# Kernel tuning notes

Measured on AMD Instinct MI355X. Metric: run time of the kernel, lower is better.

Reference implementation:

```python
import math
import jax, jax.numpy as jnp
import numpy as np

B, T, C, H = 4, 2048, 1024, 16
D = C // H          # head dim 64
FF = 4 * C          # 4096

def setup_inputs() -> dict:
    key = jax.random.key(0)
    ks = jax.random.split(key, 7)
    s = 0.02
    return {
        "x":      jax.random.normal(ks[0], (B, T, C), jnp.float32),
        "g1":     jnp.ones((C,), jnp.float32),                      # ln_1 weight (bias=False)
        "w_qkv":  jax.random.normal(ks[1], (3 * C, C), jnp.float32) * s,  # torch Linear [out,in]
        "w_o":    jax.random.normal(ks[2], (C, C), jnp.float32) * s,
        "g2":     jnp.ones((C,), jnp.float32),                      # ln_2 weight
        "w_fc":   jax.random.normal(ks[3], (FF, C), jnp.float32) * s,
        "w_proj": jax.random.normal(ks[4], (C, FF), jnp.float32) * s,
    }

def _layernorm(x, g):
    mu = jnp.mean(x, axis=-1, keepdims=True)
    var = jnp.mean(jnp.square(x - mu), axis=-1, keepdims=True)
    return (x - mu) * jax.lax.rsqrt(var + 1e-5) * g

def _attn(x, w_qkv, w_o):
    qkv = x @ w_qkv.T                                  # [B,T,3C]
    q, k, v = jnp.split(qkv, 3, axis=-1)
    q = q.reshape(B, T, H, D).transpose(0, 2, 1, 3)    # [B,H,T,D]
    k = k.reshape(B, T, H, D).transpose(0, 2, 1, 3)
    v = v.reshape(B, T, H, D).transpose(0, 2, 1, 3)
    att = jnp.einsum('bhtd,bhsd->bhts', q, k) * (1.0 / math.sqrt(D))
    mask = jnp.tril(jnp.ones((T, T), bool))
    att = jnp.where(mask, att, -jnp.inf)
    att = jax.nn.softmax(att, axis=-1)
    y = jnp.einsum('bhts,bhsd->bhtd', att, v)          # [B,H,T,D]
    y = y.transpose(0, 2, 1, 3).reshape(B, T, C)
    return y @ w_o.T

def _mlp(x, w_fc, w_proj):
    h = jax.nn.gelu(x @ w_fc.T, approximate=False)     # torch nn.GELU default = exact erf
    return h @ w_proj.T

def reference(x, g1, w_qkv, w_o, g2, w_fc, w_proj):
    x = x + _attn(_layernorm(x, g1), w_qkv, w_o)
    x = x + _mlp(_layernorm(x, g2), w_fc, w_proj)
    return x
```

## Files before the change

kernel.cpp:

```cpp
#include <hip/hip_runtime.h>

typedef __attribute__((ext_vector_type(8))) short bs8;
typedef __attribute__((ext_vector_type(4))) short bs4;
typedef __attribute__((ext_vector_type(4))) float f32x4;

__device__ __forceinline__ float b2f(short u) {
  union { unsigned int i; float f; } c;
  c.i = ((unsigned int)(unsigned short)u) << 16;
  return c.f;
}
__device__ __forceinline__ unsigned short f2bs(float f) {
  union { float f; unsigned int i; } c; c.f = f;
  unsigned int r = (c.i + 0x7FFFu + ((c.i >> 16) & 1u)) >> 16;
  return (unsigned short)r;
}
__device__ __forceinline__ void async16(const void* g, void* l) {
  __builtin_amdgcn_global_load_lds((__attribute__((address_space(1))) void*)g,
                                   (__attribute__((address_space(3))) void*)l, 16, 0, 0);
}

__device__ __forceinline__ float gelu_fast(float v) {
  const float x = v * 0.70710678118654752f;
  const float ax = fabsf(x);
  const float t = 1.0f / (1.0f + 0.3275911f * ax);
  float p = 1.061405429f;
  p = p * t - 1.453152027f;
  p = p * t + 1.421413741f;
  p = p * t - 0.284496736f;
  p = p * t + 0.254829592f;
  const float e = __expf(-ax * ax);
  float er = 1.0f - p * t * e;
  er = copysignf(er, x);
  return 0.5f * v * (1.0f + er);
}

__global__ void detect_kernel(const unsigned int* __restrict__ g1raw, int* __restrict__ flag) {
  *flag = (g1raw[0] == 0x3F800000u) ? 1 : 0;
}

struct CvtArgs {
  const void* src[7];
  unsigned short* dst[7];
  int start[8];
};
__global__ __launch_bounds__(256) void cvt_all_kernel(CvtArgs a, const int* __restrict__ flag) {
  int blk = blockIdx.x;
  int seg = 0;
  #pragma unroll
  for (int s = 1; s < 7; ++s) if (blk >= a.start[s]) seg = s;
  const int i = ((blk - a.start[seg]) * 256 + threadIdx.x) * 4;
  const void* src = a.src[seg];
  unsigned short* dst = a.dst[seg];
  if (*flag) {
    const float4 t = *(const float4*)((const float*)src + i);
    bs4 o; o[0] = f2bs(t.x); o[1] = f2bs(t.y); o[2] = f2bs(t.z); o[3] = f2bs(t.w);
    *(bs4*)(dst + i) = o;
  } else {
    *(bs4*)(dst + i) = *(const bs4*)((const unsigned short*)src + i);
  }
}

__global__ __launch_bounds__(256) void ln_kernel(const unsigned short* __restrict__ xin,
                                                 const unsigned short* __restrict__ g,
                                                 unsigned short* __restrict__ out) {
  const int row = blockIdx.x;
  const int tid = threadIdx.x;
  const size_t base = (size_t)row * 1024 + tid * 4;
  float v[4];
  const bs4 t = *(const bs4*)(xin + base);
  v[0] = b2f(t[0]); v[1] = b2f(t[1]); v[2] = b2f(t[2]); v[3] = b2f(t[3]);
  float s  = v[0] + v[1] + v[2] + v[3];
  float sq = v[0]*v[0] + v[1]*v[1] + v[2]*v[2] + v[3]*v[3];
  for (int off = 32; off > 0; off >>= 1) { s += __shfl_xor(s, off); sq += __shfl_xor(sq, off); }
  __shared__ float sm[8];
  const int wv = tid >> 6;
  if ((tid & 63) == 0) { sm[wv] = s; sm[4 + wv] = sq; }
  __syncthreads();
  s  = sm[0] + sm[1] + sm[2] + sm[3];
  sq = sm[4] + sm[5] + sm[6] + sm[7];
  const float mu = s * (1.0f / 1024.0f);
  const float rstd = rsqrtf(sq * (1.0f / 1024.0f) - mu * mu + 1e-5f);
  const bs4 gt = *(const bs4*)(g + tid * 4);
  unsigned short* op = out + base;
  #pragma unroll
  for (int i = 0; i < 4; ++i) op[i] = f2bs((v[i] - mu) * rstd * b2f(gt[i]));
}

template<int EPI>
__global__ __launch_bounds__(256, 2) void gemm_bt(const unsigned short* __restrict__ X,
                                                  const unsigned short* __restrict__ W,
                                                  const unsigned short* __restrict__ res,
                                                  void* __restrict__ out,
                                                  const int* __restrict__ flagp,
                                                  int M, int N, int K) {
  __shared__ __align__(16) unsigned short Alds[2][128 * 64];
  __shared__ __align__(16) unsigned short Blds[2][128 * 64];
  const int tid  = threadIdx.x;
  const int wave = tid >> 6, lane = tid & 63;
  const int c16 = lane & 15, q8 = (lane >> 4) * 8;
  const int wm = (wave >> 1) * 64, wn = (wave & 1) * 64;

  const int nbn = gridDim.x;
  const int d = blockIdx.y * nbn + blockIdx.x;
  const int xcd = d & 7, slot = d >> 3;
  const int cpx = (nbn * gridDim.y) >> 3;
  const int sq = xcd * (cpx >> 6) + (slot >> 6);
  const int r  = slot & 63;
  const int nsx = nbn >> 3;
  const int bn = ((sq % nsx) * 8 + (r & 7)) * 128;
  const int bm = ((sq / nsx) * 8 + (r >> 3)) * 128;

  const int sw = (c16 & 7) << 4;

  int isf32 = 0;
  if constexpr (EPI == 3) isf32 = *flagp;

  f32x4 acc[4][4] = {};

  const int srow = tid >> 3;
  const int scb  = ((tid & 7) * 16) ^ ((srow & 7) << 4);

  auto STAGE = [&](int k0, int b) {
    #pragma unroll
    for (int it = 0; it < 4; ++it) {
      const int row = it * 32 + srow;
      async16((const char*)X + ((size_t)(bm + row) * K + k0) * 2 + scb,
              (char*)&Alds[b][0] + (it * 256 + tid) * 16);
      async16((const char*)W + ((size_t)(bn + row) * K + k0) * 2 + scb,
              (char*)&Blds[b][0] + (it * 256 + tid) * 16);
    }
  };

  auto COMPUTE = [&](int b) {
    const char* Ab = (const char*)&Alds[b][0];
    const char* Bb = (const char*)&Blds[b][0];
    #pragma unroll
    for (int kk = 0; kk < 64; kk += 32) {
      bs8 af[4], bf[4];
      #pragma unroll
      for (int mi = 0; mi < 4; ++mi)
        af[mi] = *(const bs8*)(Ab + (wm + mi * 16 + c16) * 128 + (((kk + q8) * 2) ^ sw));
      #pragma unroll
      for (int ni = 0; ni < 4; ++ni)
        bf[ni] = *(const bs8*)(Bb + (wn + ni * 16 + c16) * 128 + (((kk + q8) * 2) ^ sw));
      #pragma unroll
      for (int mi = 0; mi < 4; ++mi)
        #pragma unroll
        for (int ni = 0; ni < 4; ++ni)
          acc[mi][ni] = __builtin_amdgcn_mfma_f32_16x16x32_bf16(af[mi], bf[ni], acc[mi][ni], 0, 0, 0);
    }
  };

  STAGE(0, 0);
  int cur = 0;
  for (int k0 = 0; k0 < K - 64; k0 += 64) {
    STAGE(k0 + 64, cur ^ 1);
    asm volatile("s_waitcnt vmcnt(8)" ::: "memory");
    __builtin_amdgcn_s_barrier();
    COMPUTE(cur);
    __builtin_amdgcn_s_barrier();
    cur ^= 1;
  }
  asm volatile("s_waitcnt vmcnt(0)" ::: "memory");
  __builtin_amdgcn_s_barrier();
  COMPUTE(cur);

  const int q4 = (lane >> 4) * 4;
  #pragma unroll
  for (int mi = 0; mi < 4; ++mi) {
    #pragma unroll
    for (int r2 = 0; r2 < 4; ++r2) {
      const size_t row = bm + wm + mi * 16 + q4 + r2;
      #pragma unroll
      for (int ni = 0; ni < 4; ++ni) {
        const size_t col = bn + wn + ni * 16 + c16;
        const size_t idx = row * (size_t)N + col;
        float v = acc[mi][ni][r2];
        if constexpr (EPI == 0) {
          ((unsigned short*)out)[idx] = f2bs(v);
        } else if constexpr (EPI == 1) {
          ((unsigned short*)out)[idx] = f2bs(gelu_fast(v));
        } else if constexpr (EPI == 2) {
          v += b2f(res[idx]);
          ((unsigned short*)out)[idx] = f2bs(v);
        } else {
          v += b2f(res[idx]);
          if (isf32) ((float*)out)[idx] = v;
          else       ((unsigned short*)out)[idx] = f2bs(v);
        }
      }
    }
  }
}

__global__ __launch_bounds__(256) void vtrans_kernel(const unsigned short* __restrict__ qkv,
                                                     unsigned short* __restrict__ vt) {
  constexpr int T = 2048, C3 = 3072;
  __shared__ __align__(16) unsigned short tile[64][72];
  const int tid = threadIdx.x;
  const int t0 = blockIdx.x * 64;
  const int bh = blockIdx.y; const int b = bh >> 4, h = bh & 15;
  const int r = tid >> 3, c = (tid & 7) * 8;
  #pragma unroll
  for (int it = 0; it < 2; ++it) {
    const int t = it * 32 + r;
    *(bs8*)&tile[t][c] = *(const bs8*)(qkv + ((size_t)(b * T + t0 + t)) * C3 + 2048 + h * 64 + c);
  }
  __syncthreads();
  #pragma unroll
  for (int it = 0; it < 2; ++it) {
    const int d = it * 32 + r;
    bs8 o;
    #pragma unroll
    for (int j = 0; j < 8; ++j) o[j] = (short)tile[c + j][d];
    *(bs8*)(vt + ((size_t)bh * 64 + d) * T + t0 + c) = o;
  }
}

struct KF { bs8 a[4][2]; };

__device__ __forceinline__ void ldsFrag(KF& f, const char* buf, int c16, int quad) {
  const int sw = (c16 & 7) << 4;
  #pragma unroll
  for (int g = 0; g < 4; ++g) {
    const int rowb = (g * 16 + c16) * 128 + quad * 16;
    f.a[g][0] = *(const bs8*)(buf + ((rowb) ^ sw));
    f.a[g][1] = *(const bs8*)(buf + ((rowb + 64) ^ sw));
  }
}

template<bool DO_A, bool MA, bool MB>
__device__ __forceinline__ void tile2(const char* Kb, const char* Vb, int kvbase,
                                      const bs8& qfA0, const bs8& qfA1,
                                      const bs8& qfB0, const bs8& qfB1,
                                      f32x4 (&oA)[4], f32x4 (&oB)[4],
                                      float (&lsA)[4], float (&lsB)[4],
                                      char* Pw, int qrowA, int qrowB,
                                      int c16, int quad) {
  KF kf, vf;
  ldsFrag(kf, Kb, c16, quad);
  ldsFrag(vf, Vb, c16, quad);

  f32x4 sA[4], sB[4];
  #pragma unroll
  for (int g = 0; g < 4; ++g) {
    if constexpr (DO_A) {
      f32x4 z = {};
      z = __builtin_amdgcn_mfma_f32_16x16x32_bf16(qfA0, kf.a[g][0], z, 0, 0, 0);
      sA[g] = __builtin_amdgcn_mfma_f32_16x16x32_bf16(qfA1, kf.a[g][1], z, 0, 0, 0);
    }
    f32x4 z2 = {};
    z2 = __builtin_amdgcn_mfma_f32_16x16x32_bf16(qfB0, kf.a[g][0], z2, 0, 0, 0);
    sB[g] = __builtin_amdgcn_mfma_f32_16x16x32_bf16(qfB1, kf.a[g][1], z2, 0, 0, 0);
  }

  #pragma unroll
  for (int r = 0; r < 4; ++r) {
    const int prow = quad * 4 + r;
    const int pbase = prow * 128;
    const int psw = (prow & 7) << 4;
    #pragma unroll
    for (int g = 0; g < 4; ++g) {
      const int col2 = (g * 16 + c16) * 2;
      if constexpr (DO_A) {
        float p = __expf(sA[g][r] * 0.125f - 4.0f);
        if constexpr (MA) { if (kvbase + g * 16 + c16 > qrowA + r) p = 0.f; }
        lsA[r] += p;
        *(unsigned short*)(Pw + ((pbase + col2) ^ psw)) = f2bs(p);
      }
      float p2 = __expf(sB[g][r] * 0.125f - 4.0f);
      if constexpr (MB) { if (kvbase + g * 16 + c16 > qrowB + r) p2 = 0.f; }
      lsB[r] += p2;
      *(unsigned short*)(Pw + 2048 + ((pbase + col2) ^ psw)) = f2bs(p2);
    }
  }
  asm volatile("s_waitcnt lgkmcnt(0)" ::: "memory");

  const int rsw = (c16 & 7) << 4;
  const int rbase = c16 * 128 + quad * 16;
  bs8 pA0, pA1;
  if constexpr (DO_A) {
    pA0 = *(const bs8*)(Pw + ((rbase) ^ rsw));
    pA1 = *(const bs8*)(Pw + ((rbase + 64) ^ rsw));
  }
  const bs8 pB0 = *(const bs8*)(Pw + 2048 + ((rbase) ^ rsw));
  const bs8 pB1 = *(const bs8*)(Pw + 2048 + ((rbase + 64) ^ rsw));
  #pragma unroll
  for (int g = 0; g < 4; ++g) {
    if constexpr (DO_A) {
      oA[g] = __builtin_amdgcn_mfma_f32_16x16x32_bf16(pA0, vf.a[g][0], oA[g], 0, 0, 0);
      oA[g] = __builtin_amdgcn_mfma_f32_16x16x32_bf16(pA1, vf.a[g][1], oA[g], 0, 0, 0);
    }
    oB[g] = __builtin_amdgcn_mfma_f32_16x16x32_bf16(pB0, vf.a[g][0], oB[g], 0, 0, 0);
    oB[g] = __builtin_amdgcn_mfma_f32_16x16x32_bf16(pB1, vf.a[g][1], oB[g], 0, 0, 0);
  }
}

__global__ __launch_bounds__(256) void attn_kernel(const unsigned short* __restrict__ qkv,
                                                   const unsigned short* __restrict__ vt,
                                                   unsigned short* __restrict__ y) {
  constexpr int T = 2048, C3 = 3072, CC = 1024;
  __shared__ __align__(16) unsigned short Klds[2][4096];
  __shared__ __align__(16) unsigned short Vlds[2][4096];
  __shared__ __align__(16) unsigned short Plds[4][2048];

  const int tid = threadIdx.x;
  const int wv = tid >> 6, lane = tid & 63;
  const int quad = lane >> 4, c16 = lane & 15;
  const int bh = blockIdx.x;
  const int b = bh >> 4, h = bh & 15;
  const int i = blockIdx.y;
  const int qA = i, qB = 31 - i;
  const size_t rowbase = (size_t)b * T;
  char* Pw = (char*)&Plds[wv][0];

  const int y0 = tid * 16, y1 = 4096 + tid * 16;
  const int r0 = y0 >> 7, r1 = y1 >> 7;
  const int s0 = y0 ^ ((r0 & 7) << 4);
  const int s1 = y1 ^ ((r1 & 7) << 4);
  const char* Ksrc0 = (const char*)qkv + ((size_t)(b * T) + r0) * 6144 + 2048 + h * 128 + (s0 & 127);
  const char* Ksrc1 = (const char*)qkv + ((size_t)(b * T) + r1) * 6144 + 2048 + h * 128 + (s1 & 127);
  const char* Vsrc0 = (const char*)vt + ((size_t)bh * 64 + r0) * (T * 2) + (s0 & 127);
  const char* Vsrc1 = (const char*)vt + ((size_t)bh * 64 + r1) * (T * 2) + (s1 & 127);

  auto STAGE = [&](int kt, int buf) {
    char* Kb = (char*)&Klds[buf][0];
    char* Vb = (char*)&Vlds[buf][0];
    const size_t ko = (size_t)kt * (64 * 6144);
    const int vo = kt * 128;
    async16(Ksrc0 + ko, Kb + y0);
    async16(Ksrc1 + ko, Kb + y1);
    async16(Vsrc0 + vo, Vb + y0);
    async16(Vsrc1 + vo, Vb + y1);
  };

  STAGE(0, 0);

  bs8 qfA0, qfA1, qfB0, qfB1;
  {
    const unsigned short* qpA = qkv + (rowbase + qA * 64 + wv * 16 + c16) * C3 + h * 64 + quad * 8;
    qfA0 = *(const bs8*)qpA; qfA1 = *(const bs8*)(qpA + 32);
    const unsigned short* qpB = qkv + (rowbase + qB * 64 + wv * 16 + c16) * C3 + h * 64 + quad * 8;
    qfB0 = *(const bs8*)qpB; qfB1 = *(const bs8*)(qpB + 32);
  }
  const int qrowA = qA * 64 + wv * 16 + quad * 4;
  const int qrowB = qB * 64 + wv * 16 + quad * 4;

  f32x4 oA[4] = {}, oB[4] = {};
  float lsA[4] = {}, lsB[4] = {};

  __syncthreads();

  int cur = 0, kt = 0;
  for (; kt < qA; ++kt) {
    STAGE(kt + 1, cur ^ 1);
    tile2<true, false, false>((const char*)&Klds[cur][0], (const char*)&Vlds[cur][0], kt * 64,
                              qfA0, qfA1, qfB0, qfB1, oA, oB, lsA, lsB, Pw, qrowA, qrowB, c16, quad);
    __syncthreads(); cur ^= 1;
  }
  STAGE(kt + 1, cur ^ 1);
  tile2<true, true, false>((const char*)&Klds[cur][0], (const char*)&Vlds[cur][0], kt * 64,
                           qfA0, qfA1, qfB0, qfB1, oA, oB, lsA, lsB, Pw, qrowA, qrowB, c16, quad);
  __syncthreads(); cur ^= 1; ++kt;
  for (; kt < qB; ++kt) {
    STAGE(kt + 1, cur ^ 1);
    tile2<false, false, false>((const char*)&Klds[cur][0], (const char*)&Vlds[cur][0], kt * 64,
                               qfA0, qfA1, qfB0, qfB1, oA, oB, lsA, lsB, Pw, qrowA, qrowB, c16, quad);
    __syncthreads(); cur ^= 1;
  }
  tile2<false, false, true>((const char*)&Klds[cur][0], (const char*)&Vlds[cur][0], kt * 64,
                            qfA0, qfA1, qfB0, qfB1, oA, oB, lsA, lsB, Pw, qrowA, qrowB, c16, quad);

  #pragma unroll
  for (int r = 0; r < 4; ++r) {
    for (int off = 1; off < 16; off <<= 1) {
      lsA[r] += __shfl_xor(lsA[r], off);
      lsB[r] += __shfl_xor(lsB[r], off);
    }
  }

  #pragma unroll
  for (int r = 0; r < 4; ++r) {
    const float invA = 1.0f / lsA[r];
    unsigned short* ypA = y + (rowbase + qrowA + r) * CC + h * 64 + c16;
    ypA[0]  = f2bs(oA[0][r] * invA);
    ypA[16] = f2bs(oA[1][r] * invA);
    ypA[32] = f2bs(oA[2][r] * invA);
    ypA[48] = f2bs(oA[3][r] * invA);
    const float invB = 1.0f / lsB[r];
    unsigned short* ypB = y + (rowbase + qrowB + r) * CC + h * 64 + c16;
    ypB[0]  = f2bs(oB[0][r] * invB);
    ypB[16] = f2bs(oB[1][r] * invB);
    ypB[32] = f2bs(oB[2][r] * invB);
    ypB[48] = f2bs(oB[3][r] * invB);
  }
}

extern "C" void kernel_launch(void* const* d_in, const int* in_sizes, int n_in,
                              void* d_out, int out_size, void* d_ws, size_t ws_size,
                              hipStream_t stream) {
  char* ws = (char*)d_ws;
  unsigned short* xc     = (unsigned short*)(ws);
  unsigned short* wqkvc  = (unsigned short*)(ws + 16777216);
  unsigned short* woc    = (unsigned short*)(ws + 23068672);
  unsigned short* wfcc   = (unsigned short*)(ws + 25165824);
  unsigned short* wprojc = (unsigned short*)(ws + 33554432);
  unsigned short* g1c    = (unsigned short*)(ws + 41943040);
  unsigned short* g2c    = (unsigned short*)(ws + 41945088);
  unsigned short* vt     = (unsigned short*)(ws + 41947136);
  unsigned short* x1     = (unsigned short*)(ws + 41947136);
  unsigned short* qkv    = (unsigned short*)(ws + 58724352);
  unsigned short* hb     = (unsigned short*)(ws + 58724352);
  unsigned short* xn     = (unsigned short*)(ws + 125833216);
  unsigned short* yb     = (unsigned short*)(ws + 125833216);
  int*            flag   = (int*)(ws + 142610432);

  const int M = 8192;

  detect_kernel<<<1, 1, 0, stream>>>((const unsigned int*)d_in[1], flag);

  CvtArgs ca;
  ca.src[0] = d_in[0]; ca.dst[0] = xc;     int b0 = 8192;
  ca.src[1] = d_in[1]; ca.dst[1] = g1c;    int b1 = 1;
  ca.src[2] = d_in[2]; ca.dst[2] = wqkvc;  int b2 = 3072;
  ca.src[3] = d_in[3]; ca.dst[3] = woc;    int b3 = 1024;
  ca.src[4] = d_in[4]; ca.dst[4] = g2c;    int b4 = 1;
  ca.src[5] = d_in[5]; ca.dst[5] = wfcc;   int b5 = 4096;
  ca.src[6] = d_in[6]; ca.dst[6] = wprojc; int b6 = 4096;
  ca.start[0] = 0;
  ca.start[1] = b0;
  ca.start[2] = b0 + b1;
  ca.start[3] = b0 + b1 + b2;
  ca.start[4] = b0 + b1 + b2 + b3;
  ca.start[5] = b0 + b1 + b2 + b3 + b4;
  ca.start[6] = b0 + b1 + b2 + b3 + b4 + b5;
  ca.start[7] = b0 + b1 + b2 + b3 + b4 + b5 + b6;
  cvt_all_kernel<<<ca.start[7], 256, 0, stream>>>(ca, flag);

  ln_kernel<<<M, 256, 0, stream>>>(xc, g1c, xn);
  gemm_bt<0><<<dim3(24, 64), 256, 0, stream>>>(xn, wqkvc, nullptr, qkv, nullptr, M, 3072, 1024);
  vtrans_kernel<<<dim3(32, 64), 256, 0, stream>>>(qkv, vt);
  attn_kernel<<<dim3(64, 16), 256, 0, stream>>>(qkv, vt, yb);
  gemm_bt<2><<<dim3(8, 64), 256, 0, stream>>>(yb, woc, xc, x1, nullptr, M, 1024, 1024);
  ln_kernel<<<M, 256, 0, stream>>>(x1, g2c, xn);
  gemm_bt<1><<<dim3(32, 64), 256, 0, stream>>>(xn, wfcc, nullptr, hb, nullptr, M, 4096, 1024);
  gemm_bt<3><<<dim3(8, 64), 256, 0, stream>>>(hb, wprojc, x1, d_out, flag, M, 1024, 4096);
}
```

Measured before the change: 485.3 us.

## Add 256x256-tile 512-thread GEMM with triple-buffered A for QKV and FC

Introduces a new GEMM kernel with 256x256 output tiles, 8 waves, a 3-stage LDS ring for A and 2-stage for B. Global loads are interleaved between MFMA sub-blocks, and s_setprio is raised around the MFMA bursts. It replaces the 128x128 gemm_bt for the QKV and FC projections to increase operand reuse per loaded byte and overlap loads with compute. It uses 160KB of LDS and many accumulator registers, which limits occupancy and gives fewer blocks, so the grid is coarser across CUs.

```diff
diff --git a/kernel.cpp b/kernel.cpp
--- a/kernel.cpp
+++ b/kernel.cpp
@@ -87,6 +87,143 @@
 }
 
 template<int EPI>
+__global__ __launch_bounds__(512, 2) void gemm256p(const unsigned short* __restrict__ X,
+                                                   const unsigned short* __restrict__ W,
+                                                   void* __restrict__ out,
+                                                   int M, int N, int K) {
+  __shared__ __align__(16) unsigned short Al[3][256 * 64];
+  __shared__ __align__(16) unsigned short Bl[2][256 * 64];
+  const int tid = threadIdx.x;
+  const int wv = tid >> 6, lane = tid & 63;
+  const int c16 = lane & 15, q8 = (lane >> 4) * 8;
+  const int wr = wv >> 2, wc = wv & 3;
+  const int bm = blockIdx.y * 256, bn = blockIdx.x * 256;
+  const int sw = (c16 & 7) << 4;
+
+  f32x4 acc[8][4] = {};
+
+  const int trow = tid >> 3;
+  const int scb  = ((tid & 7) * 16) ^ ((trow & 7) << 4);
+  const int ldst = tid * 16;
+  const size_t rstep = (size_t)64 * K * 2;
+
+  auto issueA = [&](int t, int u, int slot) {
+    char* dst = (char*)&Al[0][0] + slot * 32768 + u * 16384 + ldst;
+    const char* s = (const char*)X + ((size_t)(bm + u * 128 + trow) * K + t * 64) * 2 + scb;
+    async16(s, dst);
+    async16(s + rstep, dst + 8192);
+  };
+  auto issueB = [&](int t, int u, int slot) {
+    char* dst = (char*)&Bl[0][0] + slot * 32768 + u * 16384 + ldst;
+    const char* s = (const char*)W + ((size_t)(bn + u * 128 + trow) * K + t * 64) * 2 + scb;
+    async16(s, dst);
+    async16(s + rstep, dst + 8192);
+  };
+
+  issueA(0, 0, 0); issueA(0, 1, 0); issueA(1, 0, 1);
+  issueB(0, 0, 0); issueB(0, 1, 0); issueA(1, 1, 1);
+
+  const int NT = K >> 6;
+  int sa = 0, sb = 0;
+
+#define LGKM_FENCE  asm volatile("s_waitcnt lgkmcnt(0)" ::: "memory"); \
+                    __builtin_amdgcn_sched_barrier(0);
+
+  for (int t = 0; t < NT; ++t) {
+    if (t == NT - 1) { asm volatile("s_waitcnt vmcnt(0)" ::: "memory"); }
+    else             { asm volatile("s_waitcnt vmcnt(2)" ::: "memory"); }
+    __builtin_amdgcn_s_barrier();
+
+    int sa2 = sa + 2; if (sa2 >= 3) sa2 -= 3;
+    const char* Ab = (const char*)&Al[0][0] + sa * 32768;
+    const char* Bb = (const char*)&Bl[0][0] + sb * 32768;
+
+    if (t + 2 < NT) issueA(t + 2, 0, sa2);
+    bs8 bf[2][4];
+    #pragma unroll
+    for (int x = 0; x < 2; ++x)
+      #pragma unroll
+      for (int ni = 0; ni < 4; ++ni)
+        bf[x][ni] = *(const bs8*)(Bb + (wc * 64 + ni * 16 + c16) * 128 + (((x * 32 + q8) * 2) ^ sw));
+    bs8 af[4];
+    #pragma unroll
+    for (int mi = 0; mi < 4; ++mi)
+      af[mi] = *(const bs8*)(Ab + (wr * 128 + mi * 16 + c16) * 128 + ((q8 * 2) ^ sw));
+    LGKM_FENCE
+    __builtin_amdgcn_s_setprio(1);
+    #pragma unroll
+    for (int mi = 0; mi < 4; ++mi)
+      #pragma unroll
+      for (int ni = 0; ni < 4; ++ni)
+        acc[mi][ni] = __builtin_amdgcn_mfma_f32_16x16x32_bf16(af[mi], bf[0][ni], acc[mi][ni], 0, 0, 0);
+    __builtin_amdgcn_s_setprio(0);
+
+    if (t + 1 < NT) issueB(t + 1, 0, sb ^ 1);
+    #pragma unroll
+    for (int mi = 0; mi < 4; ++mi)
+      af[mi] = *(const bs8*)(Ab + (wr * 128 + 64 + mi * 16 + c16) * 128 + ((q8 * 2) ^ sw));
+    LGKM_FENCE
+    __builtin_amdgcn_s_setprio(1);
+    #pragma unroll
+    for (int mi = 0; mi < 4; ++mi)
+      #pragma unroll
+      for (int ni = 0; ni < 4; ++ni)
+        acc[4 + mi][ni] = __builtin_amdgcn_mfma_f32_16x16x32_bf16(af[mi], bf[0][ni], acc[4 + mi][ni], 0, 0, 0);
+    __builtin_amdgcn_s_setprio(0);
+
+    if (t + 1 < NT) issueB(t + 1, 1, sb ^ 1);
+    #pragma unroll
+    for (int mi = 0; mi < 4; ++mi)
+      af[mi] = *(const bs8*)(Ab + (wr * 128 + mi * 16 + c16) * 128 + (((32 + q8) * 2) ^ sw));
+    LGKM_FENCE
+    __builtin_amdgcn_s_setprio(1);
+    #pragma unroll
+    for (int mi = 0; mi < 4; ++mi)
+      #pragma unroll
+      for (int ni = 0; ni < 4; ++ni)
+        acc[mi][ni] = __builtin_amdgcn_mfma_f32_16x16x32_bf16(af[mi], bf[1][ni], acc[mi][ni], 0, 0, 0);
+    __builtin_amdgcn_s_setprio(0);
+
+    if (t + 2 < NT) issueA(t + 2, 1, sa2);
+    #pragma unroll
+    for (int mi = 0; mi < 4; ++mi)
+      af[mi] = *(const bs8*)(Ab + (wr * 128 + 64 + mi * 16 + c16) * 128 + (((32 + q8) * 2) ^ sw));
+    LGKM_FENCE
+    __builtin_amdgcn_s_setprio(1);
+    #pragma unroll
+    for (int mi = 0; mi < 4; ++mi)
+      #pragma unroll
+      for (int ni = 0; ni < 4; ++ni)
+        acc[4 + mi][ni] = __builtin_amdgcn_mfma_f32_16x16x32_bf16(af[mi], bf[1][ni], acc[4 + mi][ni], 0, 0, 0);
+    __builtin_amdgcn_s_setprio(0);
+
+    ++sa; if (sa == 3) sa = 0;
+    sb ^= 1;
+  }
+#undef LGKM_FENCE
+
+  const int q4 = (lane >> 4) * 4;
+  #pragma unroll
+  for (int am = 0; am < 8; ++am) {
+    #pragma unroll
+    for (int r = 0; r < 4; ++r) {
+      const size_t row = bm + wr * 128 + am * 16 + q4 + r;
+      #pragma unroll
+      for (int ni = 0; ni < 4; ++ni) {
+        const size_t col = bn + wc * 64 + ni * 16 + c16;
+        const size_t idx = row * (size_t)N + col;
+        float v = acc[am][ni][r];
+        if constexpr (EPI == 0) {
+          ((unsigned short*)out)[idx] = f2bs(v);
+        } else {
+          ((unsigned short*)out)[idx] = f2bs(gelu_fast(v));
+        }
+      }
+    }
+  }
+}
+
+template<int EPI>
 __global__ __launch_bounds__(256, 2) void gemm_bt(const unsigned short* __restrict__ X,
                                                   const unsigned short* __restrict__ W,
                                                   const unsigned short* __restrict__ res,
@@ -176,11 +313,7 @@
         const size_t col = bn + wn + ni * 16 + c16;
         const size_t idx = row * (size_t)N + col;
         float v = acc[mi][ni][r2];
-        if constexpr (EPI == 0) {
-          ((unsigned short*)out)[idx] = f2bs(v);
-        } else if constexpr (EPI == 1) {
-          ((unsigned short*)out)[idx] = f2bs(gelu_fast(v));
-        } else if constexpr (EPI == 2) {
+        if constexpr (EPI == 2) {
           v += b2f(res[idx]);
           ((unsigned short*)out)[idx] = f2bs(v);
         } else {
@@ -438,11 +571,11 @@
   cvt_all_kernel<<<ca.start[7], 256, 0, stream>>>(ca, flag);
 
   ln_kernel<<<M, 256, 0, stream>>>(xc, g1c, xn);
-  gemm_bt<0><<<dim3(24, 64), 256, 0, stream>>>(xn, wqkvc, nullptr, qkv, nullptr, M, 3072, 1024);
+  gemm256p<0><<<dim3(12, 32), 512, 0, stream>>>(xn, wqkvc, qkv, M, 3072, 1024);
   vtrans_kernel<<<dim3(32, 64), 256, 0, stream>>>(qkv, vt);
   attn_kernel<<<dim3(64, 16), 256, 0, stream>>>(qkv, vt, yb);
   gemm_bt<2><<<dim3(8, 64), 256, 0, stream>>>(yb, woc, xc, x1, nullptr, M, 1024, 1024);
   ln_kernel<<<M, 256, 0, stream>>>(x1, g2c, xn);
-  gemm_bt<1><<<dim3(32, 64), 256, 0, stream>>>(xn, wfcc, nullptr, hb, nullptr, M, 4096, 1024);
+  gemm256p<1><<<dim3(16, 32), 512, 0, stream>>>(xn, wfcc, hb, M, 4096, 1024);
   gemm_bt<3><<<dim3(8, 64), 256, 0, stream>>>(hb, wprojc, x1, d_out, flag, M, 1024, 4096);
 }
```

After: 519.0 us. 6.9% more time.
